# Kernel optimization log

Hardware: AMD Instinct MI355X
Metric: run time of the kernel (lower is better)

Reference implementation:

```python
import jax, jax.numpy as jnp
import numpy as np

N = 2048       # num nodes
E = 4096       # num edges
D_NODE = 128
D_EDGE = 128
H = 4          # heads
DH = D_EDGE // H
C = 16         # num classes
NODE_K = N // 2   # node_k_ratio = 0.5
EDGE_K = E // 2   # edge_k_ratio = 0.5
NEG = -1e9


def setup_inputs() -> dict:
    key = jax.random.key(0)
    ks = jax.random.split(key, 16)
    w = lambda k, shape: jax.random.normal(k, shape, jnp.float32) * 0.02
    return {
        "node_features": jax.random.normal(ks[0], (N, D_NODE), jnp.float32),
        "edge_features": jax.random.normal(ks[1], (E, D_EDGE), jnp.float32),
        "edge_index": jax.random.randint(ks[2], (2, E), 0, N, jnp.int32),
        # ImportanceRouter: scalar scores per node / edge
        "w_router_n": w(ks[3], (D_NODE,)),
        "w_router_e": w(ks[4], (D_EDGE,)),
        # EdgeAttention projections
        "w_e": w(ks[5], (D_EDGE, D_EDGE)),
        "w_n": w(ks[6], (D_NODE, D_EDGE)),
        "w_q": w(ks[7], (D_EDGE, D_EDGE)),
        "w_k": w(ks[8], (D_EDGE, D_EDGE)),
        "w_v": w(ks[9], (D_EDGE, D_EDGE)),
        "w_o": w(ks[10], (D_EDGE, D_EDGE)),
        # classifier MLP: Linear -> GELU -> Linear
        "w1": w(ks[11], (D_EDGE, D_EDGE)),
        "b1": jnp.zeros((D_EDGE,), jnp.float32),
        "w2": w(ks[12], (D_EDGE, C)),
        "b2": jnp.zeros((C,), jnp.float32),
    }


def reference(node_features, edge_features, edge_index,
              w_router_n, w_router_e,
              w_e, w_n, w_q, w_k, w_v, w_o,
              w1, b1, w2, b2):
    src, dst = edge_index[0], edge_index[1]

    # --- ImportanceRouter: node/edge scores ---
    ns = node_features @ w_router_n   # [N]
    es = edge_features @ w_router_e   # [E]

    # --- apply_top_k(node_k_ratio=0.5, edge_k_ratio=0.5) ---
    _, nidx = jax.lax.top_k(ns, NODE_K)
    node_mask = jnp.zeros((N,), bool).at[nidx].set(True)
    _, eidx = jax.lax.top_k(es, EDGE_K)
    edge_topk = jnp.zeros((E,), bool).at[eidx].set(True)
    edge_mask = edge_topk & node_mask[src] & node_mask[dst]   # [E]

    ef = edge_features * edge_mask[:, None].astype(edge_features.dtype)

    # --- build_edge_adjacency: edges sharing a node attend to each other ---
    adj = ((src[:, None] == src[None, :]) | (src[:, None] == dst[None, :]) |
           (dst[:, None] == src[None, :]) | (dst[:, None] == dst[None, :]))  # [E,E]

    # --- EdgeAttention: edge rep mixes edge feats and endpoint node feats ---
    h = ef @ w_e + (node_features[src] + node_features[dst]) @ w_n   # [E, D_EDGE]
    q = (h @ w_q).reshape(E, H, DH)
    k = (h @ w_k).reshape(E, H, DH)
    v = (h @ w_v).reshape(E, H, DH)
    scores = jnp.einsum('ehd,fhd->hef', q, k) / np.float32(np.sqrt(DH))  # [H,E,E]
    scores = jnp.where(adj[None, :, :], scores, NEG)
    attn = jax.nn.softmax(scores, axis=-1)
    o = jnp.einsum('hef,fhd->ehd', attn, v).reshape(E, D_EDGE) @ w_o    # [E, D_EDGE]

    # --- classifier: Linear -> GELU -> Linear ---
    x = jax.nn.gelu(o @ w1 + b1)
    logits = x @ w2 + b2            # [E, C]
    return logits
```

## Files before the change

kernel.cpp:

```cpp
#include <hip/hip_runtime.h>
#include <hip/hip_bf16.h>
#include <math.h>

#define NN 2048
#define NE 4096
#define D 128
#define NODE_K 1024
#define EDGE_K 2048
#define CAP 64

typedef const __hip_bfloat16* bfp;
typedef unsigned short u16;
typedef __attribute__((ext_vector_type(8))) short short8;
typedef __attribute__((ext_vector_type(4))) float floatx4;

#define MFMA16(a, b, c) __builtin_amdgcn_mfma_f32_16x16x32_bf16(a, b, c, 0, 0, 0)

__device__ __forceinline__ float b2f(__hip_bfloat16 x) { return __bfloat162float(x); }

__device__ __forceinline__ float ldx(const void* p, size_t i, int f) {
  return f ? ((const float*)p)[i] : b2f(((bfp)p)[i]);
}
__device__ __forceinline__ float4 ldx4(const void* p, size_t i4, int f) {
  if (f) return ((const float4*)p)[i4];
  ushort4 u = ((const ushort4*)p)[i4];
  float4 r;
  r.x = __uint_as_float(((unsigned)u.x) << 16);
  r.y = __uint_as_float(((unsigned)u.y) << 16);
  r.z = __uint_as_float(((unsigned)u.z) << 16);
  r.w = __uint_as_float(((unsigned)u.w) << 16);
  return r;
}

__device__ __forceinline__ void split2(float x, u16& hi, u16& lo) {
  unsigned u = __float_as_uint(x);
  unsigned h = (u + 0x7FFFu + ((u >> 16) & 1u)) >> 16;
  hi = (u16)h;
  float r = x - __uint_as_float(h << 16);
  unsigned v = __float_as_uint(r);
  lo = (u16)((v + 0x7FFFu + ((v >> 16) & 1u)) >> 16);
}
__device__ __forceinline__ void build_frags(const float* v8, short8& fh, short8& fl) {
  #pragma unroll
  for (int i = 0; i < 8; ++i) {
    u16 h, l;
    split2(v8[i], h, l);
    fh[i] = (short)h; fl[i] = (short)l;
  }
}

__device__ __forceinline__ int detect_f(const u16* raw, int* s4) {
  int t = threadIdx.x;
  int weird = 0;
  for (int i = t; i < 1024; i += blockDim.x) {
    unsigned int bits = ((unsigned int)raw[i]) << 16;
    float x = __uint_as_float(bits);
    float ax = fabsf(x);
    if (!(ax <= 1e3f) || (x != 0.f && ax < 1e-12f)) weird++;
  }
  #pragma unroll
  for (int m = 32; m >= 1; m >>= 1) weird += __shfl_xor(weird, m);
  int nw = (int)blockDim.x >> 6;
  if ((t & 63) == 0) s4[t >> 6] = weird;
  __syncthreads();
  int tot = 0;
  for (int i = 0; i < nw; ++i) tot += s4[i];
  return (tot > 50) ? 1 : 0;
}

struct K1Args {
  const void *nf, *ef, *wrn, *wre;
  const void* w[7];
  float *ns, *es;
  int *deg, *flag;
  u16 *wtHi, *wtLo;
  u16 *feHi, *feLo;
};

#define SCORE_BLOCKS ((NN + NE) / 4)
#define WPREP_BLOCKS 112
#define FSPLIT_BLOCKS 192
__global__ __launch_bounds__(256) void scores_prep_kernel(K1Args a) {
  __shared__ int s4[4];
  int b = blockIdx.x, t = threadIdx.x;
  int f = detect_f((const u16*)a.nf, s4);
  if (b < SCORE_BLOCKS) {
    int wid = b * 4 + (t >> 6), lane = t & 63;
    const void* base; const void* w; float* out; size_t r0;
    if (wid < NN) { base = a.nf; r0 = (size_t)wid * D; w = a.wrn; out = a.ns + wid; }
    else { int r = wid - NN; base = a.ef; r0 = (size_t)r * D; w = a.wre; out = a.es + r; }
    double p = (double)ldx(base, r0 + lane, f) * (double)ldx(w, lane, f)
             + (double)ldx(base, r0 + lane + 64, f) * (double)ldx(w, lane + 64, f);
    #pragma unroll
    for (int m = 32; m >= 1; m >>= 1) p += __shfl_xor(p, m);
    if (lane == 0) *out = (float)p;
  } else if (b == SCORE_BLOCKS) {
    if (t == 0) a.flag[0] = f;
    for (int i = t; i < NN; i += 256) a.deg[i] = 0;
  } else if (b <= SCORE_BLOCKS + WPREP_BLOCKS) {
    int tau = (b - SCORE_BLOCKS - 1) * 256 + t;
    int w = tau >> 12, rem = tau & 4095;
    int n = rem >> 5, k0 = (rem & 31) * 4;
    ushort4 hi, lo;
    split2(ldx(a.w[w], (size_t)(k0 + 0) * 128 + n, f), hi.x, lo.x);
    split2(ldx(a.w[w], (size_t)(k0 + 1) * 128 + n, f), hi.y, lo.y);
    split2(ldx(a.w[w], (size_t)(k0 + 2) * 128 + n, f), hi.z, lo.z);
    split2(ldx(a.w[w], (size_t)(k0 + 3) * 128 + n, f), hi.w, lo.w);
    ((ushort4*)a.wtHi)[tau] = hi;
    ((ushort4*)a.wtLo)[tau] = lo;
  } else {
    int fb = b - SCORE_BLOCKS - 1 - WPREP_BLOCKS;
    #pragma unroll
    for (int i = 0; i < 4; ++i) {
      int g4 = fb * 1024 + i * 256 + t;
      float4 x = (g4 < NN * D / 4) ? ldx4(a.nf, g4, f)
                                   : ldx4(a.ef, g4 - NN * D / 4, f);
      ushort4 hi, lo;
      split2(x.x, hi.x, lo.x);
      split2(x.y, hi.y, lo.y);
      split2(x.z, hi.z, lo.z);
      split2(x.w, hi.w, lo.w);
      ((ushort4*)a.feHi)[g4] = hi;
      ((ushort4*)a.feLo)[g4] = lo;
    }
  }
}

#define NMB (NN / 4)
#define EMB (NE / 4)
__global__ __launch_bounds__(256) void mask_lists_kernel(
    const float* __restrict__ ns, const float* __restrict__ es,
    const int* __restrict__ src, const int* __restrict__ dst,
    int* __restrict__ node_mask, int* __restrict__ edge_topk,
    int* __restrict__ deg, int* __restrict__ lists) {
  int b = blockIdx.x, t = threadIdx.x;
  if (b < NMB) {
    int i = b * 4 + (t >> 6), lane = t & 63;
    float si = ns[i];
    int rank = 0;
    for (int j4 = lane; j4 < NN / 4; j4 += 64) {
      float4 sj = ((const float4*)ns)[j4];
      int j = j4 * 4;
      rank += (sj.x > si) || (sj.x == si && j + 0 < i);
      rank += (sj.y > si) || (sj.y == si && j + 1 < i);
      rank += (sj.z > si) || (sj.z == si && j + 2 < i);
      rank += (sj.w > si) || (sj.w == si && j + 3 < i);
    }
    #pragma unroll
    for (int m = 32; m >= 1; m >>= 1) rank += __shfl_xor(rank, m);
    if (lane == 0) node_mask[i] = (rank < NODE_K) ? 1 : 0;
  } else if (b < NMB + EMB) {
    int i = (b - NMB) * 4 + (t >> 6), lane = t & 63;
    float si = es[i];
    int rank = 0;
    for (int j4 = lane; j4 < NE / 4; j4 += 64) {
      float4 sj = ((const float4*)es)[j4];
      int j = j4 * 4;
      rank += (sj.x > si) || (sj.x == si && j + 0 < i);
      rank += (sj.y > si) || (sj.y == si && j + 1 < i);
      rank += (sj.z > si) || (sj.z == si && j + 2 < i);
      rank += (sj.w > si) || (sj.w == si && j + 3 < i);
    }
    #pragma unroll
    for (int m = 32; m >= 1; m >>= 1) rank += __shfl_xor(rank, m);
    if (lane == 0) edge_topk[i] = (rank < EDGE_K) ? 1 : 0;
  } else {
    int e = (b - NMB - EMB) * 256 + t;
    if (e < NE) {
      int sn = src[e], dn = dst[e];
      int p = atomicAdd(&deg[sn], 1);
      if (p >= 0 && p < CAP) lists[sn * CAP + p] = e;
      if (dn != sn) {
        p = atomicAdd(&deg[dn], 1);
        if (p >= 0 && p < CAP) lists[dn * CAP + p] = e;
      }
    }
  }
}

__global__ __launch_bounds__(512) void h_qkv_mfma_kernel(
    const u16* __restrict__ feHi, const u16* __restrict__ feLo,
    const int* __restrict__ src, const int* __restrict__ dst,
    const int* __restrict__ node_mask, const int* __restrict__ edge_topk,
    const u16* __restrict__ wtHi, const u16* __restrict__ wtLo,
    float* __restrict__ qkv) {
  __shared__ __align__(16) float hf[8 * 64 * 4];
  int t = threadIdx.x;
  int wave = t >> 6, lane = t & 63;
  int qd = lane >> 4, c = lane & 15;
  int row0 = blockIdx.x * 16;
  int e = row0 + c;
  int sn = src[e], dn = dst[e];
  bool em = edge_topk[e] && node_mask[sn] && node_mask[dn];
  int n0 = wave * 16;
  const u16* efH = feHi + (size_t)NN * D;
  const u16* efL = feLo + (size_t)NN * D;
  const short8 z8 = {0, 0, 0, 0, 0, 0, 0, 0};

  short8 A1h[4], A1l[4], Sh[4], Sl[4], Dh[4], Dl[4];
  short8 BEh[4], BEl[4], BNh[4], BNl[4];
  #pragma unroll
  for (int ks = 0; ks < 4; ++ks) {
    int k0 = ks * 32 + qd * 8;
    A1h[ks] = *(const short8*)(efH + (size_t)e * D + k0);
    A1l[ks] = *(const short8*)(efL + (size_t)e * D + k0);
    Sh[ks]  = *(const short8*)(feHi + (size_t)sn * D + k0);
    Sl[ks]  = *(const short8*)(feLo + (size_t)sn * D + k0);
    Dh[ks]  = *(const short8*)(feHi + (size_t)dn * D + k0);
    Dl[ks]  = *(const short8*)(feLo + (size_t)dn * D + k0);
    size_t bo = (size_t)(n0 + c) * 128 + k0;
    BEh[ks] = *(const short8*)(wtHi + bo);
    BEl[ks] = *(const short8*)(wtLo + bo);
    BNh[ks] = *(const short8*)(wtHi + 16384 + bo);
    BNl[ks] = *(const short8*)(wtLo + 16384 + bo);
  }
  if (!em) {
    #pragma unroll
    for (int ks = 0; ks < 4; ++ks) { A1h[ks] = z8; A1l[ks] = z8; }
  }
  floatx4 accE = {0.f, 0.f, 0.f, 0.f};
  floatx4 accN = {0.f, 0.f, 0.f, 0.f};
  #pragma unroll
  for (int ks = 0; ks < 4; ++ks) {
    accE = MFMA16(A1h[ks], BEh[ks], accE);
    accN = MFMA16(Sh[ks], BNh[ks], accN);
    accE = MFMA16(A1l[ks], BEh[ks], accE);
    accN = MFMA16(Sl[ks], BNh[ks], accN);
    accE = MFMA16(A1h[ks], BEl[ks], accE);
    accN = MFMA16(Sh[ks], BNl[ks], accN);
    accN = MFMA16(Dh[ks], BNh[ks], accN);
    accN = MFMA16(Dl[ks], BNh[ks], accN);
    accN = MFMA16(Dh[ks], BNl[ks], accN);
  }
  {
    int np = n0 + c;
    int kd = np >> 5, qq = (np >> 3) & 3, half = (c >> 2) & 1, j4 = c & 3;
    #pragma unroll
    for (int r = 0; r < 4; ++r)
      hf[((kd * 2 + half) * 64 + qq * 16 + 4 * qd + r) * 4 + j4] = accE[r] + accN[r];
  }
  short8 BQh[4], BQl[4], BKh[4], BKl[4], BVh[4], BVl[4];
  #pragma unroll
  for (int ks = 0; ks < 4; ++ks) {
    size_t bo = (size_t)(n0 + c) * 128 + ks * 32 + qd * 8;
    BQh[ks] = *(const short8*)(wtHi + 2 * 16384 + bo);
    BQl[ks] = *(const short8*)(wtLo + 2 * 16384 + bo);
    BKh[ks] = *(const short8*)(wtHi + 3 * 16384 + bo);
    BKl[ks] = *(const short8*)(wtLo + 3 * 16384 + bo);
    BVh[ks] = *(const short8*)(wtHi + 4 * 16384 + bo);
    BVl[ks] = *(const short8*)(wtLo + 4 * 16384 + bo);
  }
  __syncthreads();
  floatx4 aq = {0.f, 0.f, 0.f, 0.f};
  floatx4 ak = {0.f, 0.f, 0.f, 0.f};
  floatx4 av = {0.f, 0.f, 0.f, 0.f};
  #pragma unroll
  for (int ks = 0; ks < 4; ++ks) {
    float4 p0 = *(const float4*)&hf[((ks * 2 + 0) * 64 + lane) * 4];
    float4 p1 = *(const float4*)&hf[((ks * 2 + 1) * 64 + lane) * 4];
    float v8[8] = {p0.x, p0.y, p0.z, p0.w, p1.x, p1.y, p1.z, p1.w};
    short8 ah, al;
    build_frags(v8, ah, al);
    aq = MFMA16(ah, BQh[ks], aq);
    ak = MFMA16(ah, BKh[ks], ak);
    av = MFMA16(ah, BVh[ks], av);
    aq = MFMA16(al, BQh[ks], aq);
    ak = MFMA16(al, BKh[ks], ak);
    av = MFMA16(al, BVh[ks], av);
    aq = MFMA16(ah, BQl[ks], aq);
    ak = MFMA16(ah, BKl[ks], ak);
    av = MFMA16(ah, BVl[ks], av);
  }
  #pragma unroll
  for (int r = 0; r < 4; ++r) {
    size_t ro = (size_t)(row0 + 4 * qd + r) * D + n0 + c;
    qkv[ro] = aq[r];
    qkv[(size_t)NE * D + ro] = ak[r];
    qkv[(size_t)2 * NE * D + ro] = av[r];
  }
}

__global__ __launch_bounds__(512) void attn_kernel(
    const float* __restrict__ q, const float* __restrict__ k,
    const float* __restrict__ v, const int* __restrict__ src,
    const int* __restrict__ dst, const int* __restrict__ deg,
    const int* __restrict__ lists, float* __restrict__ ao) {
  __shared__ float sm[4][128], sl[4][128], sa[4][128];
  int e = blockIdx.x;
  int t = threadIdx.x;
  int par = t >> 7, jj = t & 127;
  float qj = q[(size_t)e * D + jj];
  int sn = src[e], dn = dst[e];
  float m = -1e30f, l = 0.f, acc = 0.f;
  const float scale = 0.17677669529663687f;
  int degA = max(0, min(deg[sn], CAP));
  for (int i = par; i < degA; i += 4) {
    int fe = lists[sn * CAP + i];
    float p = qj * k[(size_t)fe * D + jj];
    p += __shfl_xor(p, 16); p += __shfl_xor(p, 8); p += __shfl_xor(p, 4);
    p += __shfl_xor(p, 2);  p += __shfl_xor(p, 1);
    float s = p * scale;
    float vj = v[(size_t)fe * D + jj];
    float mn = fmaxf(m, s);
    float corr = expf(m - mn);
    float w = expf(s - mn);
    l = l * corr + w;
    acc = acc * corr + w * vj;
    m = mn;
  }
  if (dn != sn) {
    int degB = max(0, min(deg[dn], CAP));
    for (int i = par; i < degB; i += 4) {
      int fe = lists[dn * CAP + i];
      if (src[fe] == sn || dst[fe] == sn) continue;
      float p = qj * k[(size_t)fe * D + jj];
      p += __shfl_xor(p, 16); p += __shfl_xor(p, 8); p += __shfl_xor(p, 4);
      p += __shfl_xor(p, 2);  p += __shfl_xor(p, 1);
      float s = p * scale;
      float vj = v[(size_t)fe * D + jj];
      float mn = fmaxf(m, s);
      float corr = expf(m - mn);
      float w = expf(s - mn);
      l = l * corr + w;
      acc = acc * corr + w * vj;
      m = mn;
    }
  }
  sm[par][jj] = m; sl[par][jj] = l; sa[par][jj] = acc;
  __syncthreads();
  if (par == 0) {
    float M = m;
    #pragma unroll
    for (int p2 = 1; p2 < 4; ++p2) M = fmaxf(M, sm[p2][jj]);
    float cs = expf(m - M);
    float L = l * cs, A = acc * cs;
    #pragma unroll
    for (int p2 = 1; p2 < 4; ++p2) {
      float c2 = expf(sm[p2][jj] - M);
      L += sl[p2][jj] * c2;
      A += sa[p2][jj] * c2;
    }
    ao[(size_t)e * D + jj] = A / fmaxf(L, 1e-37f);
  }
}

__global__ __launch_bounds__(512) void o_mlp_mfma_kernel(
    const float* __restrict__ ao,
    const u16* __restrict__ wtHi, const u16* __restrict__ wtLo,
    const void* __restrict__ b1, const void* __restrict__ w2,
    const void* __restrict__ b2, const int* __restrict__ flag,
    void* __restrict__ out) {
  __shared__ __align__(16) float hf[8 * 64 * 4];
  __shared__ __align__(16) float xl[16 * 132];
  __shared__ __align__(16) float w2t[16 * 132];
  int t = threadIdx.x;
  int wave = t >> 6, lane = t & 63;
  int qd = lane >> 4, c = lane & 15;
  int f = flag[0];
  int row0 = blockIdx.x * 16;
  int n0 = wave * 16;

  short8 BOh[4], BOl[4], B1h[4], B1l[4];
  #pragma unroll
  for (int ks = 0; ks < 4; ++ks) {
    size_t bo = (size_t)(n0 + c) * 128 + ks * 32 + qd * 8;
    BOh[ks] = *(const short8*)(wtHi + 5 * 16384 + bo);
    BOl[ks] = *(const short8*)(wtLo + 5 * 16384 + bo);
    B1h[ks] = *(const short8*)(wtHi + 6 * 16384 + bo);
    B1l[ks] = *(const short8*)(wtLo + 6 * 16384 + bo);
  }
  floatx4 acc = {0.f, 0.f, 0.f, 0.f};
  #pragma unroll
  for (int ks = 0; ks < 4; ++ks) {
    int k0 = ks * 32 + qd * 8;
    const float* ap = ao + (size_t)(row0 + c) * D + k0;
    float4 p0 = *(const float4*)ap;
    float4 p1 = *(const float4*)(ap + 4);
    float v8[8] = {p0.x, p0.y, p0.z, p0.w, p1.x, p1.y, p1.z, p1.w};
    short8 ah, al;
    build_frags(v8, ah, al);
    acc = MFMA16(ah, BOh[ks], acc);
    acc = MFMA16(al, BOh[ks], acc);
    acc = MFMA16(ah, BOl[ks], acc);
  }
  {
    int np = n0 + c;
    int kd = np >> 5, qq = (np >> 3) & 3, half = (c >> 2) & 1, j4 = c & 3;
    #pragma unroll
    for (int r = 0; r < 4; ++r)
      hf[((kd * 2 + half) * 64 + qq * 16 + 4 * qd + r) * 4 + j4] = acc[r];
  }
  __syncthreads();
  floatx4 a2c = {0.f, 0.f, 0.f, 0.f};
  #pragma unroll
  for (int ks = 0; ks < 4; ++ks) {
    float4 p0 = *(const float4*)&hf[((ks * 2 + 0) * 64 + lane) * 4];
    float4 p1 = *(const float4*)&hf[((ks * 2 + 1) * 64 + lane) * 4];
    float v8[8] = {p0.x, p0.y, p0.z, p0.w, p1.x, p1.y, p1.z, p1.w};
    short8 ah, al;
    build_frags(v8, ah, al);
    a2c = MFMA16(ah, B1h[ks], a2c);
    a2c = MFMA16(al, B1h[ks], a2c);
    a2c = MFMA16(ah, B1l[ks], a2c);
  }
  float bj = ldx(b1, n0 + c, f);
  #pragma unroll
  for (int r = 0; r < 4; ++r) {
    float u = a2c[r] + bj;
    float inner = 0.7978845608028654f * (u + 0.044715f * u * u * u);
    xl[(4 * qd + r) * 132 + n0 + c] = 0.5f * u * (1.f + tanhf(inner));
  }
  for (int i = t; i < D * 16; i += 512) {
    int kk = i >> 4, cc = i & 15;
    w2t[cc * 132 + kk] = ldx(w2, i, f);
  }
  __syncthreads();
  if (t < 256) {
    int r = t >> 4, cc = t & 15;
    const float4* xr = (const float4*)&xl[r * 132];
    const float4* wr = (const float4*)&w2t[cc * 132];
    float s = 0.f;
    #pragma unroll
    for (int k4 = 0; k4 < D / 4; ++k4) {
      float4 xa = xr[k4], wb = wr[k4];
      s += xa.x * wb.x + xa.y * wb.y + xa.z * wb.z + xa.w * wb.w;
    }
    s += ldx(b2, cc, f);
    int idx = (row0 + r) * 16 + cc;
    if (f) ((float*)out)[idx] = s;
    else ((__hip_bfloat16*)out)[idx] = __float2bfloat16(s);
  }
}

extern "C" void kernel_launch(void* const* d_in, const int* in_sizes, int n_in,
                              void* d_out, int out_size, void* d_ws, size_t ws_size,
                              hipStream_t stream) {
  const int* eidx = (const int*)d_in[2];
  const int* src = eidx;
  const int* dst = eidx + NE;

  size_t off = 0;
  char* base = (char*)d_ws;
  auto alloc = [&](size_t nbytes) -> void* {
    void* p = base + off;
    off += (nbytes + 255) & ~(size_t)255;
    return p;
  };
  int* flag      = (int*)alloc(256);
  float* ns      = (float*)alloc(NN * sizeof(float));
  float* es      = (float*)alloc(NE * sizeof(float));
  int* node_mask = (int*)alloc(NN * sizeof(int));
  int* edge_topk = (int*)alloc(NE * sizeof(int));
  int* deg       = (int*)alloc(NN * sizeof(int));
  int* lists     = (int*)alloc((size_t)NN * CAP * sizeof(int));
  u16* wtHi      = (u16*)alloc((size_t)7 * 16384 * sizeof(u16));
  u16* wtLo      = (u16*)alloc((size_t)7 * 16384 * sizeof(u16));
  u16* feHi      = (u16*)alloc((size_t)(NN + NE) * D * sizeof(u16));
  u16* feLo      = (u16*)alloc((size_t)(NN + NE) * D * sizeof(u16));
  float* qkv     = (float*)alloc((size_t)3 * NE * D * sizeof(float));
  float* ao      = (float*)alloc((size_t)NE * D * sizeof(float));
  float* qb = qkv, *kb = qkv + NE * D, *vb = qkv + 2 * NE * D;

  K1Args a1;
  a1.nf = d_in[0]; a1.ef = d_in[1]; a1.wrn = d_in[3]; a1.wre = d_in[4];
  a1.w[0] = d_in[5];  a1.w[1] = d_in[6];  a1.w[2] = d_in[7];
  a1.w[3] = d_in[8];  a1.w[4] = d_in[9];  a1.w[5] = d_in[10]; a1.w[6] = d_in[11];
  a1.ns = ns; a1.es = es; a1.deg = deg; a1.flag = flag;
  a1.wtHi = wtHi; a1.wtLo = wtLo; a1.feHi = feHi; a1.feLo = feLo;

  scores_prep_kernel<<<SCORE_BLOCKS + 1 + WPREP_BLOCKS + FSPLIT_BLOCKS, 256, 0,
                       stream>>>(a1);
  mask_lists_kernel<<<NMB + EMB + NE / 256, 256, 0, stream>>>(
      ns, es, src, dst, node_mask, edge_topk, deg, lists);
  h_qkv_mfma_kernel<<<NE / 16, 512, 0, stream>>>(
      feHi, feLo, src, dst, node_mask, edge_topk, wtHi, wtLo, qkv);
  attn_kernel<<<NE, 512, 0, stream>>>(qb, kb, vb, src, dst, deg, lists, ao);
  o_mlp_mfma_kernel<<<NE / 16, 512, 0, stream>>>(
      ao, wtHi, wtLo, d_in[12], d_in[13], d_in[14], flag, d_out);
}
```

Before: 144.9 us.

## Fuse five kernel launches into one cooperative persistent kernel with grid syncs

```diff
diff --git a/kernel.cpp b/kernel.cpp
--- a/kernel.cpp
+++ b/kernel.cpp
@@ -1,4 +1,5 @@
 #include <hip/hip_runtime.h>
+#include <hip/hip_cooperative_groups.h>
 #include <hip/hip_bf16.h>
 #include <math.h>
 
@@ -8,6 +9,8 @@
 #define NODE_K 1024
 #define EDGE_K 2048
 #define CAP 64
+#define GRID 256
+#define BLK 512
 
 typedef const __hip_bfloat16* bfp;
 typedef unsigned short u16;
@@ -49,10 +52,10 @@
   }
 }
 
-__device__ __forceinline__ int detect_f(const u16* raw, int* s4) {
+__device__ __forceinline__ int detect_f(const u16* raw, int* s8) {
   int t = threadIdx.x;
   int weird = 0;
-  for (int i = t; i < 1024; i += blockDim.x) {
+  for (int i = t; i < 1024; i += BLK) {
     unsigned int bits = ((unsigned int)raw[i]) << 16;
     float x = __uint_as_float(bits);
     float ax = fabsf(x);
@@ -60,32 +63,43 @@
   }
   #pragma unroll
   for (int m = 32; m >= 1; m >>= 1) weird += __shfl_xor(weird, m);
-  int nw = (int)blockDim.x >> 6;
-  if ((t & 63) == 0) s4[t >> 6] = weird;
+  if ((t & 63) == 0) s8[t >> 6] = weird;
   __syncthreads();
   int tot = 0;
-  for (int i = 0; i < nw; ++i) tot += s4[i];
+  #pragma unroll
+  for (int i = 0; i < BLK / 64; ++i) tot += s8[i];
   return (tot > 50) ? 1 : 0;
 }
 
-struct K1Args {
+struct FusedArgs {
   const void *nf, *ef, *wrn, *wre;
   const void* w[7];
+  const void *b1, *w2, *b2;
+  const int *src, *dst;
   float *ns, *es;
-  int *deg, *flag;
+  int *node_mask, *edge_topk, *deg, *lists;
   u16 *wtHi, *wtLo;
   u16 *feHi, *feLo;
+  float *qkv;
+  void *out;
 };
 
-#define SCORE_BLOCKS ((NN + NE) / 4)
-#define WPREP_BLOCKS 112
-#define FSPLIT_BLOCKS 192
-__global__ __launch_bounds__(256) void scores_prep_kernel(K1Args a) {
-  __shared__ int s4[4];
+__global__ __launch_bounds__(BLK, 2) void fused_kernel(FusedArgs a) {
+  namespace cg = cooperative_groups;
+  cg::grid_group grid = cg::this_grid();
+  __shared__ int s8[BLK / 64];
+  __shared__ __align__(16) float hf[8 * 64 * 4];
+  __shared__ __align__(16) float ao_lds[16 * 132];
+  __shared__ __align__(16) float xl[16 * 132];
+  __shared__ __align__(16) float w2t[16 * 132];
+
   int b = blockIdx.x, t = threadIdx.x;
-  int f = detect_f((const u16*)a.nf, s4);
-  if (b < SCORE_BLOCKS) {
-    int wid = b * 4 + (t >> 6), lane = t & 63;
+  int wave = t >> 6, lane = t & 63;
+  int gid = b * BLK + t;
+  int gw = b * 8 + wave;
+  int f = detect_f((const u16*)a.nf, s8);
+
+  for (int wid = gw; wid < NN + NE; wid += 2048) {
     const void* base; const void* w; float* out; size_t r0;
     if (wid < NN) { base = a.nf; r0 = (size_t)wid * D; w = a.wrn; out = a.ns + wid; }
     else { int r = wid - NN; base = a.ef; r0 = (size_t)r * D; w = a.wre; out = a.es + r; }
@@ -94,11 +108,9 @@
     #pragma unroll
     for (int m = 32; m >= 1; m >>= 1) p += __shfl_xor(p, m);
     if (lane == 0) *out = (float)p;
-  } else if (b == SCORE_BLOCKS) {
-    if (t == 0) a.flag[0] = f;
-    for (int i = t; i < NN; i += 256) a.deg[i] = 0;
-  } else if (b <= SCORE_BLOCKS + WPREP_BLOCKS) {
-    int tau = (b - SCORE_BLOCKS - 1) * 256 + t;
+  }
+  if (gid < 28672) {
+    int tau = gid;
     int w = tau >> 12, rem = tau & 4095;
     int n = rem >> 5, k0 = (rem & 31) * 4;
     ushort4 hi, lo;
@@ -108,327 +120,308 @@
     split2(ldx(a.w[w], (size_t)(k0 + 3) * 128 + n, f), hi.w, lo.w);
     ((ushort4*)a.wtHi)[tau] = hi;
     ((ushort4*)a.wtLo)[tau] = lo;
-  } else {
-    int fb = b - SCORE_BLOCKS - 1 - WPREP_BLOCKS;
-    #pragma unroll
-    for (int i = 0; i < 4; ++i) {
-      int g4 = fb * 1024 + i * 256 + t;
-      float4 x = (g4 < NN * D / 4) ? ldx4(a.nf, g4, f)
-                                   : ldx4(a.ef, g4 - NN * D / 4, f);
-      ushort4 hi, lo;
-      split2(x.x, hi.x, lo.x);
-      split2(x.y, hi.y, lo.y);
-      split2(x.z, hi.z, lo.z);
-      split2(x.w, hi.w, lo.w);
-      ((ushort4*)a.feHi)[g4] = hi;
-      ((ushort4*)a.feLo)[g4] = lo;
-    }
-  }
-}
-
-#define NMB (NN / 4)
-#define EMB (NE / 4)
-__global__ __launch_bounds__(256) void mask_lists_kernel(
-    const float* __restrict__ ns, const float* __restrict__ es,
-    const int* __restrict__ src, const int* __restrict__ dst,
-    int* __restrict__ node_mask, int* __restrict__ edge_topk,
-    int* __restrict__ deg, int* __restrict__ lists) {
-  int b = blockIdx.x, t = threadIdx.x;
-  if (b < NMB) {
-    int i = b * 4 + (t >> 6), lane = t & 63;
-    float si = ns[i];
+  }
+  for (int g4 = gid; g4 < (NN + NE) * D / 4; g4 += GRID * BLK) {
+    float4 x = (g4 < NN * D / 4) ? ldx4(a.nf, g4, f)
+                                 : ldx4(a.ef, g4 - NN * D / 4, f);
+    ushort4 hi, lo;
+    split2(x.x, hi.x, lo.x);
+    split2(x.y, hi.y, lo.y);
+    split2(x.z, hi.z, lo.z);
+    split2(x.w, hi.w, lo.w);
+    ((ushort4*)a.feHi)[g4] = hi;
+    ((ushort4*)a.feLo)[g4] = lo;
+  }
+  if (gid < NN) a.deg[gid] = 0;
+  grid.sync();
+
+  {
+    float si = a.ns[gw];
     int rank = 0;
     for (int j4 = lane; j4 < NN / 4; j4 += 64) {
-      float4 sj = ((const float4*)ns)[j4];
+      float4 sj = ((const float4*)a.ns)[j4];
       int j = j4 * 4;
-      rank += (sj.x > si) || (sj.x == si && j + 0 < i);
-      rank += (sj.y > si) || (sj.y == si && j + 1 < i);
-      rank += (sj.z > si) || (sj.z == si && j + 2 < i);
-      rank += (sj.w > si) || (sj.w == si && j + 3 < i);
+      rank += (sj.x > si) || (sj.x == si && j + 0 < gw);
+      rank += (sj.y > si) || (sj.y == si && j + 1 < gw);
+      rank += (sj.z > si) || (sj.z == si && j + 2 < gw);
+      rank += (sj.w > si) || (sj.w == si && j + 3 < gw);
     }
     #pragma unroll
     for (int m = 32; m >= 1; m >>= 1) rank += __shfl_xor(rank, m);
-    if (lane == 0) node_mask[i] = (rank < NODE_K) ? 1 : 0;
-  } else if (b < NMB + EMB) {
-    int i = (b - NMB) * 4 + (t >> 6), lane = t & 63;
-    float si = es[i];
-    int rank = 0;
-    for (int j4 = lane; j4 < NE / 4; j4 += 64) {
-      float4 sj = ((const float4*)es)[j4];
-      int j = j4 * 4;
-      rank += (sj.x > si) || (sj.x == si && j + 0 < i);
-      rank += (sj.y > si) || (sj.y == si && j + 1 < i);
-      rank += (sj.z > si) || (sj.z == si && j + 2 < i);
-      rank += (sj.w > si) || (sj.w == si && j + 3 < i);
-    }
-    #pragma unroll
-    for (int m = 32; m >= 1; m >>= 1) rank += __shfl_xor(rank, m);
-    if (lane == 0) edge_topk[i] = (rank < EDGE_K) ? 1 : 0;
-  } else {
-    int e = (b - NMB - EMB) * 256 + t;
-    if (e < NE) {
-      int sn = src[e], dn = dst[e];
-      int p = atomicAdd(&deg[sn], 1);
-      if (p >= 0 && p < CAP) lists[sn * CAP + p] = e;
+    if (lane == 0) a.node_mask[gw] = (rank < NODE_K) ? 1 : 0;
+    #pragma unroll
+    for (int rr = 0; rr < 2; ++rr) {
+      int i = gw + rr * 2048;
+      float se = a.es[i];
+      int rk = 0;
+      for (int j4 = lane; j4 < NE / 4; j4 += 64) {
+        float4 sj = ((const float4*)a.es)[j4];
+        int j = j4 * 4;
+        rk += (sj.x > se) || (sj.x == se && j + 0 < i);
+        rk += (sj.y > se) || (sj.y == se && j + 1 < i);
+        rk += (sj.z > se) || (sj.z == se && j + 2 < i);
+        rk += (sj.w > se) || (sj.w == se && j + 3 < i);
+      }
+      #pragma unroll
+      for (int m = 32; m >= 1; m >>= 1) rk += __shfl_xor(rk, m);
+      if (lane == 0) a.edge_topk[i] = (rk < EDGE_K) ? 1 : 0;
+    }
+    if (gid < NE) {
+      int e = gid;
+      int sn = a.src[e], dn = a.dst[e];
+      int p = atomicAdd(&a.deg[sn], 1);
+      if (p >= 0 && p < CAP) a.lists[sn * CAP + p] = e;
       if (dn != sn) {
-        p = atomicAdd(&deg[dn], 1);
-        if (p >= 0 && p < CAP) lists[dn * CAP + p] = e;
-      }
-    }
-  }
-}
-
-__global__ __launch_bounds__(512) void h_qkv_mfma_kernel(
-    const u16* __restrict__ feHi, const u16* __restrict__ feLo,
-    const int* __restrict__ src, const int* __restrict__ dst,
-    const int* __restrict__ node_mask, const int* __restrict__ edge_topk,
-    const u16* __restrict__ wtHi, const u16* __restrict__ wtLo,
-    float* __restrict__ qkv) {
-  __shared__ __align__(16) float hf[8 * 64 * 4];
-  int t = threadIdx.x;
-  int wave = t >> 6, lane = t & 63;
-  int qd = lane >> 4, c = lane & 15;
-  int row0 = blockIdx.x * 16;
-  int e = row0 + c;
-  int sn = src[e], dn = dst[e];
-  bool em = edge_topk[e] && node_mask[sn] && node_mask[dn];
-  int n0 = wave * 16;
-  const u16* efH = feHi + (size_t)NN * D;
-  const u16* efL = feLo + (size_t)NN * D;
-  const short8 z8 = {0, 0, 0, 0, 0, 0, 0, 0};
-
-  short8 A1h[4], A1l[4], Sh[4], Sl[4], Dh[4], Dl[4];
-  short8 BEh[4], BEl[4], BNh[4], BNl[4];
-  #pragma unroll
-  for (int ks = 0; ks < 4; ++ks) {
-    int k0 = ks * 32 + qd * 8;
-    A1h[ks] = *(const short8*)(efH + (size_t)e * D + k0);
-    A1l[ks] = *(const short8*)(efL + (size_t)e * D + k0);
-    Sh[ks]  = *(const short8*)(feHi + (size_t)sn * D + k0);
-    Sl[ks]  = *(const short8*)(feLo + (size_t)sn * D + k0);
-    Dh[ks]  = *(const short8*)(feHi + (size_t)dn * D + k0);
-    Dl[ks]  = *(const short8*)(feLo + (size_t)dn * D + k0);
-    size_t bo = (size_t)(n0 + c) * 128 + k0;
-    BEh[ks] = *(const short8*)(wtHi + bo);
-    BEl[ks] = *(const short8*)(wtLo + bo);
-    BNh[ks] = *(const short8*)(wtHi + 16384 + bo);
-    BNl[ks] = *(const short8*)(wtLo + 16384 + bo);
-  }
-  if (!em) {
-    #pragma unroll
-    for (int ks = 0; ks < 4; ++ks) { A1h[ks] = z8; A1l[ks] = z8; }
-  }
-  floatx4 accE = {0.f, 0.f, 0.f, 0.f};
-  floatx4 accN = {0.f, 0.f, 0.f, 0.f};
-  #pragma unroll
-  for (int ks = 0; ks < 4; ++ks) {
-    accE = MFMA16(A1h[ks], BEh[ks], accE);
-    accN = MFMA16(Sh[ks], BNh[ks], accN);
-    accE = MFMA16(A1l[ks], BEh[ks], accE);
-    accN = MFMA16(Sl[ks], BNh[ks], accN);
-    accE = MFMA16(A1h[ks], BEl[ks], accE);
-    accN = MFMA16(Sh[ks], BNl[ks], accN);
-    accN = MFMA16(Dh[ks], BNh[ks], accN);
-    accN = MFMA16(Dl[ks], BNh[ks], accN);
-    accN = MFMA16(Dh[ks], BNl[ks], accN);
-  }
+        p = atomicAdd(&a.deg[dn], 1);
+        if (p >= 0 && p < CAP) a.lists[dn * CAP + p] = e;
+      }
+    }
+  }
+  grid.sync();
+
+  int row0 = b * 16;
   {
-    int np = n0 + c;
-    int kd = np >> 5, qq = (np >> 3) & 3, half = (c >> 2) & 1, j4 = c & 3;
-    #pragma unroll
-    for (int r = 0; r < 4; ++r)
-      hf[((kd * 2 + half) * 64 + qq * 16 + 4 * qd + r) * 4 + j4] = accE[r] + accN[r];
-  }
-  short8 BQh[4], BQl[4], BKh[4], BKl[4], BVh[4], BVl[4];
-  #pragma unroll
-  for (int ks = 0; ks < 4; ++ks) {
-    size_t bo = (size_t)(n0 + c) * 128 + ks * 32 + qd * 8;
-    BQh[ks] = *(const short8*)(wtHi + 2 * 16384 + bo);
-    BQl[ks] = *(const short8*)(wtLo + 2 * 16384 + bo);
-    BKh[ks] = *(const short8*)(wtHi + 3 * 16384 + bo);
-    BKl[ks] = *(const short8*)(wtLo + 3 * 16384 + bo);
-    BVh[ks] = *(const short8*)(wtHi + 4 * 16384 + bo);
-    BVl[ks] = *(const short8*)(wtLo + 4 * 16384 + bo);
+    int qd = lane >> 4, c = lane & 15;
+    int e = row0 + c;
+    int sn = a.src[e], dn = a.dst[e];
+    bool em = a.edge_topk[e] && a.node_mask[sn] && a.node_mask[dn];
+    int n0 = wave * 16;
+    const u16* efH = a.feHi + (size_t)NN * D;
+    const u16* efL = a.feLo + (size_t)NN * D;
+    const short8 z8 = {0, 0, 0, 0, 0, 0, 0, 0};
+
+    short8 A1h[4], A1l[4], Sh[4], Sl[4], Dh[4], Dl[4];
+    short8 BEh[4], BEl[4], BNh[4], BNl[4];
+    #pragma unroll
+    for (int ks = 0; ks < 4; ++ks) {
+      int k0 = ks * 32 + qd * 8;
+      A1h[ks] = *(const short8*)(efH + (size_t)e * D + k0);
+      A1l[ks] = *(const short8*)(efL + (size_t)e * D + k0);
+      Sh[ks]  = *(const short8*)(a.feHi + (size_t)sn * D + k0);
+      Sl[ks]  = *(const short8*)(a.feLo + (size_t)sn * D + k0);
+      Dh[ks]  = *(const short8*)(a.feHi + (size_t)dn * D + k0);
+      Dl[ks]  = *(const short8*)(a.feLo + (size_t)dn * D + k0);
+      size_t bo = (size_t)(n0 + c) * 128 + k0;
+      BEh[ks] = *(const short8*)(a.wtHi + bo);
+      BEl[ks] = *(const short8*)(a.wtLo + bo);
+      BNh[ks] = *(const short8*)(a.wtHi + 16384 + bo);
+      BNl[ks] = *(const short8*)(a.wtLo + 16384 + bo);
+    }
+    if (!em) {
+      #pragma unroll
+      for (int ks = 0; ks < 4; ++ks) { A1h[ks] = z8; A1l[ks] = z8; }
+    }
+    floatx4 accE = {0.f, 0.f, 0.f, 0.f};
+    floatx4 accN = {0.f, 0.f, 0.f, 0.f};
+    #pragma unroll
+    for (int ks = 0; ks < 4; ++ks) {
+      accE = MFMA16(A1h[ks], BEh[ks], accE);
+      accN = MFMA16(Sh[ks], BNh[ks], accN);
+      accE = MFMA16(A1l[ks], BEh[ks], accE);
+      accN = MFMA16(Sl[ks], BNh[ks], accN);
+      accE = MFMA16(A1h[ks], BEl[ks], accE);
+      accN = MFMA16(Sh[ks], BNl[ks], accN);
+      accN = MFMA16(Dh[ks], BNh[ks], accN);
+      accN = MFMA16(Dl[ks], BNh[ks], accN);
+      accN = MFMA16(Dh[ks], BNl[ks], accN);
+    }
+    {
+      int np = n0 + c;
+      int kd = np >> 5, qq = (np >> 3) & 3, half = (c >> 2) & 1, j4 = c & 3;
+      #pragma unroll
+      for (int r = 0; r < 4; ++r)
+        hf[((kd * 2 + half) * 64 + qq * 16 + 4 * qd + r) * 4 + j4] = accE[r] + accN[r];
+    }
+    short8 BQh[4], BQl[4], BKh[4], BKl[4], BVh[4], BVl[4];
+    #pragma unroll
+    for (int ks = 0; ks < 4; ++ks) {
+      size_t bo = (size_t)(n0 + c) * 128 + ks * 32 + qd * 8;
+      BQh[ks] = *(const short8*)(a.wtHi + 2 * 16384 + bo);
+      BQl[ks] = *(const short8*)(a.wtLo + 2 * 16384 + bo);
+      BKh[ks] = *(const short8*)(a.wtHi + 3 * 16384 + bo);
+      BKl[ks] = *(const short8*)(a.wtLo + 3 * 16384 + bo);
+      BVh[ks] = *(const short8*)(a.wtHi + 4 * 16384 + bo);
+      BVl[ks] = *(const short8*)(a.wtLo + 4 * 16384 + bo);
+    }
+    __syncthreads();
+    floatx4 aq = {0.f, 0.f, 0.f, 0.f};
+    floatx4 ak = {0.f, 0.f, 0.f, 0.f};
+    floatx4 av = {0.f, 0.f, 0.f, 0.f};
+    #pragma unroll
+    for (int ks = 0; ks < 4; ++ks) {
+      float4 p0 = *(const float4*)&hf[((ks * 2 + 0) * 64 + lane) * 4];
+      float4 p1 = *(const float4*)&hf[((ks * 2 + 1) * 64 + lane) * 4];
+      float v8[8] = {p0.x, p0.y, p0.z, p0.w, p1.x, p1.y, p1.z, p1.w};
+      short8 ah, al;
+      build_frags(v8, ah, al);
+      aq = MFMA16(ah, BQh[ks], aq);
+      ak = MFMA16(ah, BKh[ks], ak);
+      av = MFMA16(ah, BVh[ks], av);
+      aq = MFMA16(al, BQh[ks], aq);
+      ak = MFMA16(al, BKh[ks], ak);
+      av = MFMA16(al, BVh[ks], av);
+      aq = MFMA16(ah, BQl[ks], aq);
+      ak = MFMA16(ah, BKl[ks], ak);
+      av = MFMA16(ah, BVl[ks], av);
+    }
+    #pragma unroll
+    for (int r = 0; r < 4; ++r) {
+      size_t ro = (size_t)(row0 + 4 * qd + r) * D + n0 + c;
+      a.qkv[ro] = aq[r];
+      a.qkv[(size_t)NE * D + ro] = ak[r];
+      a.qkv[(size_t)2 * NE * D + ro] = av[r];
+    }
+  }
+  grid.sync();
+
+  {
+    const float* qb = a.qkv;
+    const float* kb = a.qkv + (size_t)NE * D;
+    const float* vb = a.qkv + (size_t)2 * NE * D;
+    int half = lane >> 5, l5 = lane & 31;
+    int el = wave * 2 + half;
+    int e = row0 + el;
+    int sn = a.src[e], dn = a.dst[e];
+    const float scale = 0.17677669529663687f;
+    float q4[4], m[4], lsum[4], acc[4];
+    #pragma unroll
+    for (int h = 0; h < 4; ++h) {
+      q4[h] = qb[(size_t)e * D + l5 + 32 * h];
+      m[h] = -1e30f; lsum[h] = 0.f; acc[h] = 0.f;
+    }
+    int degA = max(0, min(a.deg[sn], CAP));
+    for (int i = 0; i < degA; ++i) {
+      int fe = a.lists[sn * CAP + i];
+      float p[4], vv[4];
+      #pragma unroll
+      for (int h = 0; h < 4; ++h) {
+        p[h]  = q4[h] * kb[(size_t)fe * D + l5 + 32 * h];
+        vv[h] = vb[(size_t)fe * D + l5 + 32 * h];
+      }
+      #pragma unroll
+      for (int mk = 16; mk >= 1; mk >>= 1) {
+        #pragma unroll
+        for (int h = 0; h < 4; ++h) p[h] += __shfl_xor(p[h], mk);
+      }
+      #pragma unroll
+      for (int h = 0; h < 4; ++h) {
+        float s = p[h] * scale;
+        float mn = fmaxf(m[h], s);
+        float corr = expf(m[h] - mn);
+        float w = expf(s - mn);
+        lsum[h] = lsum[h] * corr + w;
+        acc[h] = acc[h] * corr + w * vv[h];
+        m[h] = mn;
+      }
+    }
+    if (dn != sn) {
+      int degB = max(0, min(a.deg[dn], CAP));
+      for (int i = 0; i < degB; ++i) {
+        int fe = a.lists[dn * CAP + i];
+        if (a.src[fe] == sn || a.dst[fe] == sn) continue;
+        float p[4], vv[4];
+        #pragma unroll
+        for (int h = 0; h < 4; ++h) {
+          p[h]  = q4[h] * kb[(size_t)fe * D + l5 + 32 * h];
+          vv[h] = vb[(size_t)fe * D + l5 + 32 * h];
+        }
+        #pragma unroll
+        for (int mk = 16; mk >= 1; mk >>= 1) {
+          #pragma unroll
+          for (int h = 0; h < 4; ++h) p[h] += __shfl_xor(p[h], mk);
+        }
+        #pragma unroll
+        for (int h = 0; h < 4; ++h) {
+          float s = p[h] * scale;
+          float mn = fmaxf(m[h], s);
+          float corr = expf(m[h] - mn);
+          float w = expf(s - mn);
+          lsum[h] = lsum[h] * corr + w;
+          acc[h] = acc[h] * corr + w * vv[h];
+          m[h] = mn;
+        }
+      }
+    }
+    #pragma unroll
+    for (int h = 0; h < 4; ++h)
+      ao_lds[el * 132 + l5 + 32 * h] = acc[h] / fmaxf(lsum[h], 1e-37f);
   }
   __syncthreads();
-  floatx4 aq = {0.f, 0.f, 0.f, 0.f};
-  floatx4 ak = {0.f, 0.f, 0.f, 0.f};
-  floatx4 av = {0.f, 0.f, 0.f, 0.f};
-  #pragma unroll
-  for (int ks = 0; ks < 4; ++ks) {
-    float4 p0 = *(const float4*)&hf[((ks * 2 + 0) * 64 + lane) * 4];
-    float4 p1 = *(const float4*)&hf[((ks * 2 + 1) * 64 + lane) * 4];
-    float v8[8] = {p0.x, p0.y, p0.z, p0.w, p1.x, p1.y, p1.z, p1.w};
-    short8 ah, al;
-    build_frags(v8, ah, al);
-    aq = MFMA16(ah, BQh[ks], aq);
-    ak = MFMA16(ah, BKh[ks], ak);
-    av = MFMA16(ah, BVh[ks], av);
-    aq = MFMA16(al, BQh[ks], aq);
-    ak = MFMA16(al, BKh[ks], ak);
-    av = MFMA16(al, BVh[ks], av);
-    aq = MFMA16(ah, BQl[ks], aq);
-    ak = MFMA16(ah, BKl[ks], ak);
-    av = MFMA16(ah, BVl[ks], av);
-  }
-  #pragma unroll
-  for (int r = 0; r < 4; ++r) {
-    size_t ro = (size_t)(row0 + 4 * qd + r) * D + n0 + c;
-    qkv[ro] = aq[r];
-    qkv[(size_t)NE * D + ro] = ak[r];
-    qkv[(size_t)2 * NE * D + ro] = av[r];
-  }
-}
-
-__global__ __launch_bounds__(512) void attn_kernel(
-    const float* __restrict__ q, const float* __restrict__ k,
-    const float* __restrict__ v, const int* __restrict__ src,
-    const int* __restrict__ dst, const int* __restrict__ deg,
-    const int* __restrict__ lists, float* __restrict__ ao) {
-  __shared__ float sm[4][128], sl[4][128], sa[4][128];
-  int e = blockIdx.x;
-  int t = threadIdx.x;
-  int par = t >> 7, jj = t & 127;
-  float qj = q[(size_t)e * D + jj];
-  int sn = src[e], dn = dst[e];
-  float m = -1e30f, l = 0.f, acc = 0.f;
-  const float scale = 0.17677669529663687f;
-  int degA = max(0, min(deg[sn], CAP));
-  for (int i = par; i < degA; i += 4) {
-    int fe = lists[sn * CAP + i];
-    float p = qj * k[(size_t)fe * D + jj];
-    p += __shfl_xor(p, 16); p += __shfl_xor(p, 8); p += __shfl_xor(p, 4);
-    p += __shfl_xor(p, 2);  p += __shfl_xor(p, 1);
-    float s = p * scale;
-    float vj = v[(size_t)fe * D + jj];
-    float mn = fmaxf(m, s);
-    float corr = expf(m - mn);
-    float w = expf(s - mn);
-    l = l * corr + w;
-    acc = acc * corr + w * vj;
-    m = mn;
-  }
-  if (dn != sn) {
-    int degB = max(0, min(deg[dn], CAP));
-    for (int i = par; i < degB; i += 4) {
-      int fe = lists[dn * CAP + i];
-      if (src[fe] == sn || dst[fe] == sn) continue;
-      float p = qj * k[(size_t)fe * D + jj];
-      p += __shfl_xor(p, 16); p += __shfl_xor(p, 8); p += __shfl_xor(p, 4);
-      p += __shfl_xor(p, 2);  p += __shfl_xor(p, 1);
-      float s = p * scale;
-      float vj = v[(size_t)fe * D + jj];
-      float mn = fmaxf(m, s);
-      float corr = expf(m - mn);
-      float w = expf(s - mn);
-      l = l * corr + w;
-      acc = acc * corr + w * vj;
-      m = mn;
-    }
-  }
-  sm[par][jj] = m; sl[par][jj] = l; sa[par][jj] = acc;
-  __syncthreads();
-  if (par == 0) {
-    float M = m;
-    #pragma unroll
-    for (int p2 = 1; p2 < 4; ++p2) M = fmaxf(M, sm[p2][jj]);
-    float cs = expf(m - M);
-    float L = l * cs, A = acc * cs;
-    #pragma unroll
-    for (int p2 = 1; p2 < 4; ++p2) {
-      float c2 = expf(sm[p2][jj] - M);
-      L += sl[p2][jj] * c2;
-      A += sa[p2][jj] * c2;
-    }
-    ao[(size_t)e * D + jj] = A / fmaxf(L, 1e-37f);
-  }
-}
-
-__global__ __launch_bounds__(512) void o_mlp_mfma_kernel(
-    const float* __restrict__ ao,
-    const u16* __restrict__ wtHi, const u16* __restrict__ wtLo,
-    const void* __restrict__ b1, const void* __restrict__ w2,
-    const void* __restrict__ b2, const int* __restrict__ flag,
-    void* __restrict__ out) {
-  __shared__ __align__(16) float hf[8 * 64 * 4];
-  __shared__ __align__(16) float xl[16 * 132];
-  __shared__ __align__(16) float w2t[16 * 132];
-  int t = threadIdx.x;
-  int wave = t >> 6, lane = t & 63;
-  int qd = lane >> 4, c = lane & 15;
-  int f = flag[0];
-  int row0 = blockIdx.x * 16;
-  int n0 = wave * 16;
-
-  short8 BOh[4], BOl[4], B1h[4], B1l[4];
-  #pragma unroll
-  for (int ks = 0; ks < 4; ++ks) {
-    size_t bo = (size_t)(n0 + c) * 128 + ks * 32 + qd * 8;
-    BOh[ks] = *(const short8*)(wtHi + 5 * 16384 + bo);
-    BOl[ks] = *(const short8*)(wtLo + 5 * 16384 + bo);
-    B1h[ks] = *(const short8*)(wtHi + 6 * 16384 + bo);
-    B1l[ks] = *(const short8*)(wtLo + 6 * 16384 + bo);
-  }
-  floatx4 acc = {0.f, 0.f, 0.f, 0.f};
-  #pragma unroll
-  for (int ks = 0; ks < 4; ++ks) {
-    int k0 = ks * 32 + qd * 8;
-    const float* ap = ao + (size_t)(row0 + c) * D + k0;
-    float4 p0 = *(const float4*)ap;
-    float4 p1 = *(const float4*)(ap + 4);
-    float v8[8] = {p0.x, p0.y, p0.z, p0.w, p1.x, p1.y, p1.z, p1.w};
-    short8 ah, al;
-    build_frags(v8, ah, al);
-    acc = MFMA16(ah, BOh[ks], acc);
-    acc = MFMA16(al, BOh[ks], acc);
-    acc = MFMA16(ah, BOl[ks], acc);
-  }
+
   {
-    int np = n0 + c;
-    int kd = np >> 5, qq = (np >> 3) & 3, half = (c >> 2) & 1, j4 = c & 3;
-    #pragma unroll
-    for (int r = 0; r < 4; ++r)
-      hf[((kd * 2 + half) * 64 + qq * 16 + 4 * qd + r) * 4 + j4] = acc[r];
-  }
-  __syncthreads();
-  floatx4 a2c = {0.f, 0.f, 0.f, 0.f};
-  #pragma unroll
-  for (int ks = 0; ks < 4; ++ks) {
-    float4 p0 = *(const float4*)&hf[((ks * 2 + 0) * 64 + lane) * 4];
-    float4 p1 = *(const float4*)&hf[((ks * 2 + 1) * 64 + lane) * 4];
-    float v8[8] = {p0.x, p0.y, p0.z, p0.w, p1.x, p1.y, p1.z, p1.w};
-    short8 ah, al;
-    build_frags(v8, ah, al);
-    a2c = MFMA16(ah, B1h[ks], a2c);
-    a2c = MFMA16(al, B1h[ks], a2c);
-    a2c = MFMA16(ah, B1l[ks], a2c);
-  }
-  float bj = ldx(b1, n0 + c, f);
-  #pragma unroll
-  for (int r = 0; r < 4; ++r) {
-    float u = a2c[r] + bj;
-    float inner = 0.7978845608028654f * (u + 0.044715f * u * u * u);
-    xl[(4 * qd + r) * 132 + n0 + c] = 0.5f * u * (1.f + tanhf(inner));
-  }
-  for (int i = t; i < D * 16; i += 512) {
-    int kk = i >> 4, cc = i & 15;
-    w2t[cc * 132 + kk] = ldx(w2, i, f);
-  }
-  __syncthreads();
-  if (t < 256) {
-    int r = t >> 4, cc = t & 15;
-    const float4* xr = (const float4*)&xl[r * 132];
-    const float4* wr = (const float4*)&w2t[cc * 132];
-    float s = 0.f;
-    #pragma unroll
-    for (int k4 = 0; k4 < D / 4; ++k4) {
-      float4 xa = xr[k4], wb = wr[k4];
-      s += xa.x * wb.x + xa.y * wb.y + xa.z * wb.z + xa.w * wb.w;
-    }
-    s += ldx(b2, cc, f);
-    int idx = (row0 + r) * 16 + cc;
-    if (f) ((float*)out)[idx] = s;
-    else ((__hip_bfloat16*)out)[idx] = __float2bfloat16(s);
+    int qd = lane >> 4, c = lane & 15;
+    int n0 = wave * 16;
+    short8 BOh[4], BOl[4], B1h[4], B1l[4];
+    #pragma unroll
+    for (int ks = 0; ks < 4; ++ks) {
+      size_t bo = (size_t)(n0 + c) * 128 + ks * 32 + qd * 8;
+      BOh[ks] = *(const short8*)(a.wtHi + 5 * 16384 + bo);
+      BOl[ks] = *(const short8*)(a.wtLo + 5 * 16384 + bo);
+      B1h[ks] = *(const short8*)(a.wtHi + 6 * 16384 + bo);
+      B1l[ks] = *(const short8*)(a.wtLo + 6 * 16384 + bo);
+    }
+    floatx4 acc = {0.f, 0.f, 0.f, 0.f};
+    #pragma unroll
+    for (int ks = 0; ks < 4; ++ks) {
+      int k0 = ks * 32 + qd * 8;
+      const float* ap = &ao_lds[c * 132 + k0];
+      float4 p0 = *(const float4*)ap;
+      float4 p1 = *(const float4*)(ap + 4);
+      float v8[8] = {p0.x, p0.y, p0.z, p0.w, p1.x, p1.y, p1.z, p1.w};
+      short8 ah, al;
+      build_frags(v8, ah, al);
+      acc = MFMA16(ah, BOh[ks], acc);
+      acc = MFMA16(al, BOh[ks], acc);
+      acc = MFMA16(ah, BOl[ks], acc);
+    }
+    __syncthreads();
+    {
+      int np = n0 + c;
+      int kd = np >> 5, qq = (np >> 3) & 3, half = (c >> 2) & 1, j4 = c & 3;
+      #pragma unroll
+      for (int r = 0; r < 4; ++r)
+        hf[((kd * 2 + half) * 64 + qq * 16 + 4 * qd + r) * 4 + j4] = acc[r];
+    }
+    __syncthreads();
+    floatx4 a2c = {0.f, 0.f, 0.f, 0.f};
+    #pragma unroll
+    for (int ks = 0; ks < 4; ++ks) {
+      float4 p0 = *(const float4*)&hf[((ks * 2 + 0) * 64 + lane) * 4];
+      float4 p1 = *(const float4*)&hf[((ks * 2 + 1) * 64 + lane) * 4];
+      float v8[8] = {p0.x, p0.y, p0.z, p0.w, p1.x, p1.y, p1.z, p1.w};
+      short8 ah, al;
+      build_frags(v8, ah, al);
+      a2c = MFMA16(ah, B1h[ks], a2c);
+      a2c = MFMA16(al, B1h[ks], a2c);
+      a2c = MFMA16(ah, B1l[ks], a2c);
+    }
+    float bj = ldx(a.b1, n0 + c, f);
+    #pragma unroll
+    for (int r = 0; r < 4; ++r) {
+      float u = a2c[r] + bj;
+      float inner = 0.7978845608028654f * (u + 0.044715f * u * u * u);
+      xl[(4 * qd + r) * 132 + n0 + c] = 0.5f * u * (1.f + tanhf(inner));
+    }
+    for (int i = t; i < D * 16; i += BLK) {
+      int kk = i >> 4, cc = i & 15;
+      w2t[cc * 132 + kk] = ldx(a.w2, i, f);
+    }
+    __syncthreads();
+    if (t < 256) {
+      int r = t >> 4, cc = t & 15;
+      const float4* xr = (const float4*)&xl[r * 132];
+      const float4* wr = (const float4*)&w2t[cc * 132];
+      float s = 0.f;
+      #pragma unroll
+      for (int k4 = 0; k4 < D / 4; ++k4) {
+        float4 xa = xr[k4], wb = wr[k4];
+        s += xa.x * wb.x + xa.y * wb.y + xa.z * wb.z + xa.w * wb.w;
+      }
+      s += ldx(a.b2, cc, f);
+      int idx = (row0 + r) * 16 + cc;
+      if (f) ((float*)a.out)[idx] = s;
+      else ((__hip_bfloat16*)a.out)[idx] = __float2bfloat16(s);
+    }
   }
 }
 
@@ -436,8 +429,6 @@
                               void* d_out, int out_size, void* d_ws, size_t ws_size,
                               hipStream_t stream) {
   const int* eidx = (const int*)d_in[2];
-  const int* src = eidx;
-  const int* dst = eidx + NE;
 
   size_t off = 0;
   char* base = (char*)d_ws;
@@ -446,7 +437,6 @@
     off += (nbytes + 255) & ~(size_t)255;
     return p;
   };
-  int* flag      = (int*)alloc(256);
   float* ns      = (float*)alloc(NN * sizeof(float));
   float* es      = (float*)alloc(NE * sizeof(float));
   int* node_mask = (int*)alloc(NN * sizeof(int));
@@ -458,23 +448,20 @@
   u16* feHi      = (u16*)alloc((size_t)(NN + NE) * D * sizeof(u16));
   u16* feLo      = (u16*)alloc((size_t)(NN + NE) * D * sizeof(u16));
   float* qkv     = (float*)alloc((size_t)3 * NE * D * sizeof(float));
-  float* ao      = (float*)alloc((size_t)NE * D * sizeof(float));
-  float* qb = qkv, *kb = qkv + NE * D, *vb = qkv + 2 * NE * D;
-
-  K1Args a1;
-  a1.nf = d_in[0]; a1.ef = d_in[1]; a1.wrn = d_in[3]; a1.wre = d_in[4];
-  a1.w[0] = d_in[5];  a1.w[1] = d_in[6];  a1.w[2] = d_in[7];
-  a1.w[3] = d_in[8];  a1.w[4] = d_in[9];  a1.w[5] = d_in[10]; a1.w[6] = d_in[11];
-  a1.ns = ns; a1.es = es; a1.deg = deg; a1.flag = flag;
-  a1.wtHi = wtHi; a1.wtLo = wtLo; a1.feHi = feHi; a1.feLo = feLo;
-
-  scores_prep_kernel<<<SCORE_BLOCKS + 1 + WPREP_BLOCKS + FSPLIT_BLOCKS, 256, 0,
-                       stream>>>(a1);
-  mask_lists_kernel<<<NMB + EMB + NE / 256, 256, 0, stream>>>(
-      ns, es, src, dst, node_mask, edge_topk, deg, lists);
-  h_qkv_mfma_kernel<<<NE / 16, 512, 0, stream>>>(
-      feHi, feLo, src, dst, node_mask, edge_topk, wtHi, wtLo, qkv);
-  attn_kernel<<<NE, 512, 0, stream>>>(qb, kb, vb, src, dst, deg, lists, ao);
-  o_mlp_mfma_kernel<<<NE / 16, 512, 0, stream>>>(
-      ao, wtHi, wtLo, d_in[12], d_in[13], d_in[14], flag, d_out);
-}
+
+  FusedArgs fa;
+  fa.nf = d_in[0]; fa.ef = d_in[1]; fa.wrn = d_in[3]; fa.wre = d_in[4];
+  fa.w[0] = d_in[5];  fa.w[1] = d_in[6];  fa.w[2] = d_in[7];
+  fa.w[3] = d_in[8];  fa.w[4] = d_in[9];  fa.w[5] = d_in[10]; fa.w[6] = d_in[11];
+  fa.b1 = d_in[12]; fa.w2 = d_in[13]; fa.b2 = d_in[14];
+  fa.src = eidx; fa.dst = eidx + NE;
+  fa.ns = ns; fa.es = es;
+  fa.node_mask = node_mask; fa.edge_topk = edge_topk;
+  fa.deg = deg; fa.lists = lists;
+  fa.wtHi = wtHi; fa.wtLo = wtLo; fa.feHi = feHi; fa.feLo = feLo;
+  fa.qkv = qkv;
+  fa.out = d_out;
+
+  void* kargs[] = {(void*)&fa};
+  hipLaunchCooperativeKernel(fused_kernel, dim3(GRID), dim3(BLK), kargs, 0, stream);
+}
```

New measurement: 263.3 us. +81.7%, slower.
